# Kernel tuning notes

Measured on AMD Instinct MI355X. Metric: run time of the kernel, lower is better.

Reference implementation:

```python
import jax, jax.numpy as jnp
import numpy as np

D_ATT = 1024
N_HEADS = 16
D_HEAD = D_ATT // N_HEADS


def _xavier(key, shape, scale):
    # xavier_uniform for Linear(d, d): limit = sqrt(6/(fan_in+fan_out))
    limit = float(np.sqrt(6.0 / (shape[0] + shape[1])))
    return jax.random.uniform(key, shape, jnp.float32, -limit, limit) * scale


def setup_inputs() -> dict:
    key = jax.random.key(0)
    ks = jax.random.split(key, 7)
    B, Lt, Ls = 2, 2048, 2048
    s = 1.0 / np.sqrt(D_ATT)
    return {
        "x_target": jax.random.normal(ks[0], (B, Lt, D_ATT), jnp.float32),
        "x_source": jax.random.normal(ks[1], (B, Ls, D_ATT), jnp.float32),
        "Wq": _xavier(ks[2], (D_ATT, D_ATT), s),  # torch Linear weight [out, in]
        "Wk": _xavier(ks[3], (D_ATT, D_ATT), s),
        "Wv": _xavier(ks[4], (D_ATT, D_ATT), s),
        "Wo": _xavier(ks[5], (D_ATT, D_ATT), 1.0),
        "bo": jax.random.uniform(ks[6], (D_ATT,), jnp.float32, -s, s),
    }


def reference(x_target, x_source, Wq, Wk, Wv, Wo, bo):
    B, Lt, _ = x_target.shape
    Ls = x_source.shape[1]
    H, Dh = N_HEADS, D_HEAD
    # projections (torch Linear: x @ W^T); RoPE defaults to identity
    Q = (x_target @ Wq.T).reshape(B, Lt, H, Dh)  # [B, Lt, H, Dh]
    K = (x_source @ Wk.T).reshape(B, Ls, H, Dh)
    V = (x_source @ Wv.T).reshape(B, Ls, H, Dh)
    scores = jnp.einsum("bthd,bshd->bhts", Q, K) / np.sqrt(Dh)
    attn = jax.nn.softmax(scores, axis=-1)
    out = jnp.einsum("bhts,bshd->bthd", attn, V).reshape(B, Lt, H * Dh)
    return out @ Wo.T + bo  # dropout p=0 -> identity
```

## Files before the change

kernel.cpp:

```cpp
#include <hip/hip_runtime.h>
#include <hip/hip_bf16.h>

typedef short bf16x8 __attribute__((ext_vector_type(8)));
typedef float f32x4 __attribute__((ext_vector_type(4)));

#define LDP 72

__device__ __forceinline__ float bf2f(ushort u) {
    union { unsigned int i; float f; } v; v.i = ((unsigned int)u) << 16; return v.f;
}
__device__ __forceinline__ ushort f2bf(float f) {
    union { float f; unsigned int i; } v; v.f = f;
    unsigned int x = v.i;
    x += 0x7fffu + ((x >> 16) & 1u);
    return (ushort)(x >> 16);
}

#define MFMA(a, b, c) __builtin_amdgcn_mfma_f32_16x16x32_bf16(a, b, c, 0, 0, 0)

#define WAIT_BARRIER(N) asm volatile("s_waitcnt vmcnt(" #N ")\n\ts_barrier" ::: "memory")

__device__ __forceinline__ void gld_lds16(const ushort* g, ushort* l) {
    __builtin_amdgcn_global_load_lds(
        (const __attribute__((address_space(1))) unsigned int*)g,
        (__attribute__((address_space(3))) unsigned int*)l, 16, 0, 0);
}

#define WS_XT 0
#define WS_XS 4194304
#define WS_WQ 8388608
#define WS_WK 9437184
#define WS_WV 10485760
#define WS_WO 11534336
#define WS_QH 12582912
#define WS_KH 16777216
#define WS_VT 20971520
#define WS_AO 0

__global__ __launch_bounds__(256) void cast_bf16(
    const float* __restrict__ s0, const float* __restrict__ s1,
    const float* __restrict__ s2, const float* __restrict__ s3,
    const float* __restrict__ s4, const float* __restrict__ s5,
    ushort* __restrict__ ws)
{
    const int seg = blockIdx.y;
    const float* src = seg == 0 ? s0 : seg == 1 ? s1 : seg == 2 ? s2
                     : seg == 3 ? s3 : seg == 4 ? s4 : s5;
    const size_t off = seg == 0 ? WS_XT : seg == 1 ? WS_XS : seg == 2 ? WS_WQ
                     : seg == 3 ? WS_WK : seg == 4 ? WS_WV : (size_t)WS_WO;
    const int n4 = (seg < 2) ? 1048576 : 262144;
    ushort* d = ws + off;
    for (int i = blockIdx.x * 256 + threadIdx.x; i < n4; i += gridDim.x * 256) {
        float4 f = ((const float4*)src)[i];
        ushort4 u;
        u.x = f2bf(f.x); u.y = f2bf(f.y); u.z = f2bf(f.z); u.w = f2bf(f.w);
        ((ushort4*)d)[i] = u;
    }
}

__global__ __launch_bounds__(256) void gemm128(
    const ushort* __restrict__ xtb, const ushort* __restrict__ xsb,
    const ushort* __restrict__ wqb, const ushort* __restrict__ wkb,
    const ushort* __restrict__ wvb,
    ushort* __restrict__ qh, ushort* __restrict__ kh, ushort* __restrict__ vt)
{
    __shared__ __align__(16) ushort SM[24576];

    const int mode = blockIdx.z;
    const ushort* Ap = (mode == 0) ? xtb : xsb;
    const ushort* Wp = (mode == 0) ? wqb : (mode == 1 ? wkb : wvb);

    const int tid  = threadIdx.x;
    const int wave = tid >> 6, lane = tid & 63;
    const int quad = lane >> 4, lidx = lane & 15;
    const int wm = wave >> 1, wn = wave & 1;
    const int m0 = blockIdx.y * 128, n0 = blockIdx.x * 128;

    const int slr = lane >> 2, scb = lane & 3;
    auto stage = [&](int k0, int bufi) {
        ushort* Asb = SM + bufi * 4096;
        ushort* Bsb = SM + 12288 + bufi * 4096;
#pragma unroll
        for (int i2 = 0; i2 < 2; ++i2) {
            const int i = wave + i2 * 4;
            const int r = i * 16 + slr;
            gld_lds16(Ap + (size_t)(m0 + r) * 1024 + k0 + scb * 8, Asb + i * 512);
            gld_lds16(Wp + (size_t)(n0 + r) * 1024 + k0 + scb * 8, Bsb + i * 512);
        }
    };

    f32x4 acc[4][4] = {};
    stage(0, 0);
    stage(32, 1);

    for (int kt = 0; kt < 32; ++kt) {
        const int cur = kt % 3;
        WAIT_BARRIER(4);
        stage(((kt + 2) & 31) * 32, (kt + 2) % 3);
        const ushort* Asb = SM + cur * 4096;
        const ushort* Bsb = SM + 12288 + cur * 4096;
        bf16x8 af[4], bfr[4];
#pragma unroll
        for (int i = 0; i < 4; ++i) {
            af[i]  = *(const bf16x8*)(Asb + (wm * 64 + i * 16 + lidx) * 32 + quad * 8);
            bfr[i] = *(const bf16x8*)(Bsb + (wn * 64 + i * 16 + lidx) * 32 + quad * 8);
        }
#pragma unroll
        for (int mi = 0; mi < 4; ++mi)
#pragma unroll
            for (int ni = 0; ni < 4; ++ni)
                acc[mi][ni] = MFMA(af[mi], bfr[ni], acc[mi][ni]);
    }
    __syncthreads();

    ushort* scr = SM + wave * 4096;

    if (mode == 2) {
#pragma unroll
        for (int mi = 0; mi < 4; ++mi)
#pragma unroll
            for (int ni = 0; ni < 4; ++ni)
#pragma unroll
                for (int r = 0; r < 4; ++r) {
                    const int dl = ni * 16 + lidx;
                    const int tl = mi * 16 + quad * 4 + r;
                    const int col = (((tl >> 3) ^ (dl & 7)) << 3) | (tl & 7);
                    scr[dl * 64 + col] = f2bf(acc[mi][ni][r]);
                }
        asm volatile("s_waitcnt lgkmcnt(0)" ::: "memory");
        const int hh = (n0 + wn * 64) >> 6;
        const int bb = m0 >> 11;
        const int t0 = (m0 + wm * 64) & 2047;
        ushort* Vtp = vt + (size_t)(bb * 16 + hh) * 64 * 2048;
#pragma unroll
        for (int ii = 0; ii < 8; ++ii) {
            const int dl = ii * 8 + (lane >> 3);
            const int tb = lane & 7;
            uint4 vd = *(const uint4*)(scr + dl * 64 + ((tb ^ (dl & 7)) << 3));
            *(uint4*)(Vtp + (size_t)dl * 2048 + t0 + tb * 8) = vd;
        }
        return;
    }

#pragma unroll
    for (int mi = 0; mi < 4; ++mi)
#pragma unroll
        for (int ni = 0; ni < 4; ++ni)
#pragma unroll
            for (int r = 0; r < 4; ++r) {
                const int tl = mi * 16 + quad * 4 + r;
                const int dl = ni * 16 + lidx;
                const int col = (((dl >> 3) ^ (tl & 7)) << 3) | (dl & 7);
                scr[tl * 64 + col] = f2bf(acc[mi][ni][r]);
            }
    asm volatile("s_waitcnt lgkmcnt(0)" ::: "memory");
    {
        ushort* dst = (mode == 0) ? qh : kh;
        const int hh = (n0 + wn * 64) >> 6;
        const int bb = m0 >> 11;
        const int tbase = (m0 + wm * 64) & 2047;
        ushort* Hp = dst + (size_t)(bb * 16 + hh) * 2048 * 64;
#pragma unroll
        for (int ii = 0; ii < 8; ++ii) {
            const int tl = ii * 8 + (lane >> 3);
            const int c  = lane & 7;
            uint4 vd = *(const uint4*)(scr + tl * 64 + ((c ^ (tl & 7)) << 3));
            *(uint4*)(Hp + (size_t)(tbase + tl) * 64 + c * 8) = vd;
        }
    }
}

__global__ __launch_bounds__(256) void gemm_out(
    const ushort* __restrict__ aob, const ushort* __restrict__ wob,
    const float* __restrict__ bias, float* __restrict__ outf)
{
    __shared__ __align__(16) ushort SM[18432];

    const int tid  = threadIdx.x;
    const int wave = tid >> 6, lane = tid & 63;
    const int quad = lane >> 4, lidx = lane & 15;
    const int m0 = blockIdx.y * 128, n0 = blockIdx.x * 64;

    const int slr = lane >> 2, scb = lane & 3;
    auto stage = [&](int k0, int bufi) {
        ushort* Asb = SM + bufi * 4096;
        ushort* Bsb = SM + 12288 + bufi * 2048;
#pragma unroll
        for (int i2 = 0; i2 < 2; ++i2) {
            const int i = wave * 2 + i2;
            gld_lds16(aob + (size_t)(m0 + i * 16 + slr) * 1024 + k0 + scb * 8,
                      Asb + i * 512);
        }
        gld_lds16(wob + (size_t)(n0 + wave * 16 + slr) * 1024 + k0 + scb * 8,
                  Bsb + wave * 512);
    };

    f32x4 acc[2][4] = {};
    stage(0, 0);
    stage(32, 1);

    for (int kt = 0; kt < 32; ++kt) {
        const int cur = kt % 3;
        WAIT_BARRIER(3);
        stage(((kt + 2) & 31) * 32, (kt + 2) % 3);
        const ushort* Asb = SM + cur * 4096;
        const ushort* Bsb = SM + 12288 + cur * 2048;
        bf16x8 af[2], bfr[4];
#pragma unroll
        for (int i = 0; i < 2; ++i)
            af[i] = *(const bf16x8*)(Asb + (wave * 32 + i * 16 + lidx) * 32 + quad * 8);
#pragma unroll
        for (int i = 0; i < 4; ++i)
            bfr[i] = *(const bf16x8*)(Bsb + (i * 16 + lidx) * 32 + quad * 8);
#pragma unroll
        for (int mi = 0; mi < 2; ++mi)
#pragma unroll
            for (int ni = 0; ni < 4; ++ni)
                acc[mi][ni] = MFMA(af[mi], bfr[ni], acc[mi][ni]);
    }

#pragma unroll
    for (int mi = 0; mi < 2; ++mi)
#pragma unroll
        for (int ni = 0; ni < 4; ++ni)
#pragma unroll
            for (int r = 0; r < 4; ++r) {
                const int m = m0 + wave * 32 + mi * 16 + quad * 4 + r;
                const int n = n0 + ni * 16 + lidx;
                outf[(size_t)m * 1024 + n] = acc[mi][ni][r] + bias[n];
            }
}

__global__ __launch_bounds__(512) void flash_attn(
    const ushort* __restrict__ Qh, const ushort* __restrict__ Kh,
    const ushort* __restrict__ Vt, ushort* __restrict__ AO)
{
    __shared__ __align__(16) ushort Kb[3][4096];
    __shared__ __align__(16) ushort Vb[3][4096];
    __shared__ __align__(16) ushort P[8][16][LDP];

    const int tid  = threadIdx.x;
    const int wave = tid >> 6, lane = tid & 63;
    const int quad = lane >> 4, lidx = lane & 15;
    const int bh = blockIdx.y;
    const int b = bh >> 4, h = bh & 15;
    const int qbase = blockIdx.x * 128 + wave * 16;

    const ushort* Qp = Qh + (size_t)bh * 2048 * 64;
    const ushort* Kp = Kh + (size_t)bh * 2048 * 64;
    const ushort* Vp = Vt + (size_t)bh * 64 * 2048;

    bf16x8 q0, q1;
    {
        const ushort* qr = Qp + (size_t)(qbase + lidx) * 64 + quad * 8;
        union { ushort u[8]; uint4 v; } t0, t1;
        t0.v = *(const uint4*)qr;
        t1.v = *(const uint4*)(qr + 32);
#pragma unroll
        for (int i = 0; i < 8; ++i) {
            ((short*)&q0)[i] = (short)f2bf(bf2f(t0.u[i]) * 0.18033688f);
            ((short*)&q1)[i] = (short)f2bf(bf2f(t1.u[i]) * 0.18033688f);
        }
    }

    auto stage = [&](int s0, int bufi) {
        const int slot = wave * 64 + lane;
        const int r  = slot >> 3;
        const int bb = slot & 7;
        const int gb = bb ^ (r & 7);
        gld_lds16(Kp + (size_t)(s0 + r) * 64 + gb * 8, &Kb[bufi][wave * 512]);
        gld_lds16(Vp + (size_t)r * 2048 + s0 + gb * 8, &Vb[bufi][wave * 512]);
    };

    float lsum = 0.f;
    f32x4 o[4] = {};

    stage(0, 0);
    stage(64, 1);

    for (int j = 0; j < 32; ++j) {
        const int cur = j % 3;
        WAIT_BARRIER(2);
        stage(((j + 2) & 31) * 64, (j + 2) % 3);

        f32x4 s[4] = {};
#pragma unroll
        for (int n0 = 0; n0 < 4; ++n0) {
            const int row = n0 * 16 + lidx;
            bf16x8 kA = *(const bf16x8*)&Kb[cur][row * 64 + ((quad ^ (row & 7)) * 8)];
            bf16x8 kB = *(const bf16x8*)&Kb[cur][row * 64 + (((4 + quad) ^ (row & 7)) * 8)];
            s[n0] = MFMA(kA, q0, s[n0]);
            s[n0] = MFMA(kB, q1, s[n0]);
        }

        bf16x8 v0[4], v1[4];
#pragma unroll
        for (int n0 = 0; n0 < 4; ++n0) {
            const int d = n0 * 16 + lidx;
            v0[n0] = *(const bf16x8*)&Vb[cur][d * 64 + ((quad ^ (d & 7)) * 8)];
            v1[n0] = *(const bf16x8*)&Vb[cur][d * 64 + (((4 + quad) ^ (d & 7)) * 8)];
        }

#pragma unroll
        for (int n0 = 0; n0 < 4; ++n0) {
            float p0 = __builtin_amdgcn_exp2f(s[n0][0]);
            float p1 = __builtin_amdgcn_exp2f(s[n0][1]);
            float p2 = __builtin_amdgcn_exp2f(s[n0][2]);
            float p3 = __builtin_amdgcn_exp2f(s[n0][3]);
            lsum += (p0 + p1) + (p2 + p3);
            uint u0, u1;
            asm("v_cvt_pk_bf16_f32 %0, %1, %2" : "=v"(u0) : "v"(p0), "v"(p1));
            asm("v_cvt_pk_bf16_f32 %0, %1, %2" : "=v"(u1) : "v"(p2), "v"(p3));
            union { uint u[2]; uint2 v; } pw;
            pw.u[0] = u0; pw.u[1] = u1;
            *(uint2*)&P[wave][lidx][n0 * 16 + quad * 4] = pw.v;
        }
        asm volatile("s_waitcnt lgkmcnt(0)" ::: "memory");

        bf16x8 pA = *(const bf16x8*)&P[wave][lidx][quad * 8];
        bf16x8 pB = *(const bf16x8*)&P[wave][lidx][32 + quad * 8];

#pragma unroll
        for (int n0 = 0; n0 < 4; ++n0) {
            o[n0] = MFMA(pA, v0[n0], o[n0]);
            o[n0] = MFMA(pB, v1[n0], o[n0]);
        }
    }

    {
        float v = lsum;
        v += __shfl_xor(v, 16);
        v += __shfl_xor(v, 32);
        lsum = v;
    }
    float rs[4];
#pragma unroll
    for (int r = 0; r < 4; ++r)
        rs[r] = 1.0f / __shfl(lsum, quad * 4 + r);

#pragma unroll
    for (int n0 = 0; n0 < 4; ++n0)
#pragma unroll
        for (int r = 0; r < 4; ++r) {
            const int tt = qbase + quad * 4 + r;
            const int d  = n0 * 16 + lidx;
            AO[(size_t)(b * 2048 + tt) * 1024 + h * 64 + d] =
                f2bf(o[n0][r] * rs[r]);
        }
}

extern "C" void kernel_launch(void* const* d_in, const int* in_sizes, int n_in,
                              void* d_out, int out_size, void* d_ws, size_t ws_size,
                              hipStream_t stream) {
    const float* xt = (const float*)d_in[0];
    const float* xs = (const float*)d_in[1];
    const float* Wq = (const float*)d_in[2];
    const float* Wk = (const float*)d_in[3];
    const float* Wv = (const float*)d_in[4];
    const float* Wo = (const float*)d_in[5];
    const float* bo = (const float*)d_in[6];
    float* out = (float*)d_out;

    ushort* ws = (ushort*)d_ws;

    cast_bf16<<<dim3(1024, 6, 1), 256, 0, stream>>>(xt, xs, Wq, Wk, Wv, Wo, ws);

    gemm128<<<dim3(8, 32, 3), 256, 0, stream>>>(
        ws + WS_XT, ws + WS_XS, ws + WS_WQ, ws + WS_WK, ws + WS_WV,
        ws + WS_QH, ws + WS_KH, ws + WS_VT);

    flash_attn<<<dim3(16, 32, 1), 512, 0, stream>>>(
        ws + WS_QH, ws + WS_KH, ws + WS_VT, ws + WS_AO);

    gemm_out<<<dim3(16, 32, 1), 256, 0, stream>>>(
        ws + WS_AO, ws + WS_WO, bo, out);
}
```

Baseline: 201.8 us.

## Switch flash attention to 32x32x16 MFMA with in-register P via permlane32 swap

Rewrites the attention inner loop to use 32x32x16 bf16 MFMA tiles, giving each of four waves 32 query rows instead of eight waves with 16 rows each. The softmax probabilities are rearranged into the A-operand layout with permlane32_swap rather than a round trip through shared memory, which removes the P LDS buffer and its lgkm wait. The block shrinks to 256 threads and each thread issues two staging loads per buffer. The cost is higher register pressure from 16-wide accumulators and fewer waves per block to hide latency.

Result: no change. 202.2 us (+0.2%).

```diff
diff --git a/kernel.cpp b/kernel.cpp
--- a/kernel.cpp
+++ b/kernel.cpp
@@ -3,8 +3,8 @@
 
 typedef short bf16x8 __attribute__((ext_vector_type(8)));
 typedef float f32x4 __attribute__((ext_vector_type(4)));
-
-#define LDP 72
+typedef float f32x16 __attribute__((ext_vector_type(16)));
+typedef unsigned int uint2v __attribute__((ext_vector_type(2)));
 
 __device__ __forceinline__ float bf2f(ushort u) {
     union { unsigned int i; float f; } v; v.i = ((unsigned int)u) << 16; return v.f;
@@ -17,6 +17,7 @@
 }
 
 #define MFMA(a, b, c) __builtin_amdgcn_mfma_f32_16x16x32_bf16(a, b, c, 0, 0, 0)
+#define MFMA32(a, b, c) __builtin_amdgcn_mfma_f32_32x32x16_bf16(a, b, c, 0, 0, 0)
 
 #define WAIT_BARRIER(N) asm volatile("s_waitcnt vmcnt(" #N ")\n\ts_barrier" ::: "memory")
 
@@ -231,121 +232,128 @@
             }
 }
 
-__global__ __launch_bounds__(512) void flash_attn(
+__global__ __launch_bounds__(256) void flash_attn(
     const ushort* __restrict__ Qh, const ushort* __restrict__ Kh,
     const ushort* __restrict__ Vt, ushort* __restrict__ AO)
 {
     __shared__ __align__(16) ushort Kb[3][4096];
     __shared__ __align__(16) ushort Vb[3][4096];
-    __shared__ __align__(16) ushort P[8][16][LDP];
 
     const int tid  = threadIdx.x;
     const int wave = tid >> 6, lane = tid & 63;
-    const int quad = lane >> 4, lidx = lane & 15;
+    const int l31 = lane & 31, hf = lane >> 5;
     const int bh = blockIdx.y;
     const int b = bh >> 4, h = bh & 15;
-    const int qbase = blockIdx.x * 128 + wave * 16;
+    const int qbase = blockIdx.x * 128 + wave * 32;
 
     const ushort* Qp = Qh + (size_t)bh * 2048 * 64;
     const ushort* Kp = Kh + (size_t)bh * 2048 * 64;
     const ushort* Vp = Vt + (size_t)bh * 64 * 2048;
 
-    bf16x8 q0, q1;
-    {
-        const ushort* qr = Qp + (size_t)(qbase + lidx) * 64 + quad * 8;
-        union { ushort u[8]; uint4 v; } t0, t1;
-        t0.v = *(const uint4*)qr;
-        t1.v = *(const uint4*)(qr + 32);
-#pragma unroll
-        for (int i = 0; i < 8; ++i) {
-            ((short*)&q0)[i] = (short)f2bf(bf2f(t0.u[i]) * 0.18033688f);
-            ((short*)&q1)[i] = (short)f2bf(bf2f(t1.u[i]) * 0.18033688f);
-        }
+    bf16x8 q[4];
+#pragma unroll
+    for (int dblk = 0; dblk < 4; ++dblk) {
+        const ushort* qr = Qp + (size_t)(qbase + l31) * 64 + dblk * 16 + hf * 8;
+        union { ushort u[8]; uint4 v; } t;
+        t.v = *(const uint4*)qr;
+#pragma unroll
+        for (int i = 0; i < 8; ++i)
+            ((short*)&q[dblk])[i] = (short)f2bf(bf2f(t.u[i]) * 0.18033688f);
     }
 
     auto stage = [&](int s0, int bufi) {
-        const int slot = wave * 64 + lane;
-        const int r  = slot >> 3;
-        const int bb = slot & 7;
-        const int gb = bb ^ (r & 7);
-        gld_lds16(Kp + (size_t)(s0 + r) * 64 + gb * 8, &Kb[bufi][wave * 512]);
-        gld_lds16(Vp + (size_t)r * 2048 + s0 + gb * 8, &Vb[bufi][wave * 512]);
+#pragma unroll
+        for (int i = 0; i < 2; ++i) {
+            const int slot = i * 256 + wave * 64 + lane;
+            const int r  = slot >> 3;
+            const int bb = slot & 7;
+            const int gb = bb ^ (r & 7);
+            gld_lds16(Kp + (size_t)(s0 + r) * 64 + gb * 8,
+                      &Kb[bufi][i * 2048 + wave * 512]);
+            gld_lds16(Vp + (size_t)r * 2048 + s0 + gb * 8,
+                      &Vb[bufi][i * 2048 + wave * 512]);
+        }
     };
 
     float lsum = 0.f;
-    f32x4 o[4] = {};
+    f32x16 o[2] = {};
 
     stage(0, 0);
     stage(64, 1);
 
     for (int j = 0; j < 32; ++j) {
         const int cur = j % 3;
-        WAIT_BARRIER(2);
+        WAIT_BARRIER(4);
         stage(((j + 2) & 31) * 64, (j + 2) % 3);
 
-        f32x4 s[4] = {};
-#pragma unroll
-        for (int n0 = 0; n0 < 4; ++n0) {
-            const int row = n0 * 16 + lidx;
-            bf16x8 kA = *(const bf16x8*)&Kb[cur][row * 64 + ((quad ^ (row & 7)) * 8)];
-            bf16x8 kB = *(const bf16x8*)&Kb[cur][row * 64 + (((4 + quad) ^ (row & 7)) * 8)];
-            s[n0] = MFMA(kA, q0, s[n0]);
-            s[n0] = MFMA(kB, q1, s[n0]);
-        }
-
-        bf16x8 v0[4], v1[4];
-#pragma unroll
-        for (int n0 = 0; n0 < 4; ++n0) {
-            const int d = n0 * 16 + lidx;
-            v0[n0] = *(const bf16x8*)&Vb[cur][d * 64 + ((quad ^ (d & 7)) * 8)];
-            v1[n0] = *(const bf16x8*)&Vb[cur][d * 64 + (((4 + quad) ^ (d & 7)) * 8)];
-        }
-
-#pragma unroll
-        for (int n0 = 0; n0 < 4; ++n0) {
-            float p0 = __builtin_amdgcn_exp2f(s[n0][0]);
-            float p1 = __builtin_amdgcn_exp2f(s[n0][1]);
-            float p2 = __builtin_amdgcn_exp2f(s[n0][2]);
-            float p3 = __builtin_amdgcn_exp2f(s[n0][3]);
-            lsum += (p0 + p1) + (p2 + p3);
-            uint u0, u1;
-            asm("v_cvt_pk_bf16_f32 %0, %1, %2" : "=v"(u0) : "v"(p0), "v"(p1));
-            asm("v_cvt_pk_bf16_f32 %0, %1, %2" : "=v"(u1) : "v"(p2), "v"(p3));
-            union { uint u[2]; uint2 v; } pw;
-            pw.u[0] = u0; pw.u[1] = u1;
-            *(uint2*)&P[wave][lidx][n0 * 16 + quad * 4] = pw.v;
-        }
-        asm volatile("s_waitcnt lgkmcnt(0)" ::: "memory");
-
-        bf16x8 pA = *(const bf16x8*)&P[wave][lidx][quad * 8];
-        bf16x8 pB = *(const bf16x8*)&P[wave][lidx][32 + quad * 8];
-
-#pragma unroll
-        for (int n0 = 0; n0 < 4; ++n0) {
-            o[n0] = MFMA(pA, v0[n0], o[n0]);
-            o[n0] = MFMA(pB, v1[n0], o[n0]);
-        }
-    }
-
-    {
-        float v = lsum;
-        v += __shfl_xor(v, 16);
-        v += __shfl_xor(v, 32);
-        lsum = v;
-    }
-    float rs[4];
-#pragma unroll
-    for (int r = 0; r < 4; ++r)
-        rs[r] = 1.0f / __shfl(lsum, quad * 4 + r);
-
-#pragma unroll
-    for (int n0 = 0; n0 < 4; ++n0)
-#pragma unroll
-        for (int r = 0; r < 4; ++r) {
-            const int tt = qbase + quad * 4 + r;
-            const int d  = n0 * 16 + lidx;
+        f32x16 s[2] = {};
+#pragma unroll
+        for (int kb = 0; kb < 2; ++kb) {
+            const int row = kb * 32 + l31;
+#pragma unroll
+            for (int dblk = 0; dblk < 4; ++dblk) {
+                bf16x8 kf = *(const bf16x8*)
+                    &Kb[cur][row * 64 + (((dblk * 2 + hf) ^ (row & 7)) * 8)];
+                s[kb] = MFMA32(kf, q[dblk], s[kb]);
+            }
+        }
+
+        bf16x8 vf[2][4];
+#pragma unroll
+        for (int db = 0; db < 2; ++db) {
+            const int drow = db * 32 + l31;
+#pragma unroll
+            for (int c = 0; c < 4; ++c)
+                vf[db][c] = *(const bf16x8*)
+                    &Vb[cur][drow * 64 + (((c * 2 + hf) ^ (drow & 7)) * 8)];
+        }
+
+        uint W[2][4][2];
+#pragma unroll
+        for (int kb = 0; kb < 2; ++kb)
+#pragma unroll
+            for (int g = 0; g < 4; ++g) {
+                float p0 = __builtin_amdgcn_exp2f(s[kb][4 * g + 0]);
+                float p1 = __builtin_amdgcn_exp2f(s[kb][4 * g + 1]);
+                float p2 = __builtin_amdgcn_exp2f(s[kb][4 * g + 2]);
+                float p3 = __builtin_amdgcn_exp2f(s[kb][4 * g + 3]);
+                lsum += (p0 + p1) + (p2 + p3);
+                asm("v_cvt_pk_bf16_f32 %0, %1, %2"
+                    : "=v"(W[kb][g][0]) : "v"(p0), "v"(p1));
+                asm("v_cvt_pk_bf16_f32 %0, %1, %2"
+                    : "=v"(W[kb][g][1]) : "v"(p2), "v"(p3));
+            }
+
+#pragma unroll
+        for (int c = 0; c < 4; ++c) {
+            const int kb = c >> 1, gL = (c & 1) * 2;
+            uint2v r0 = __builtin_amdgcn_permlane32_swap(
+                W[kb][gL][0], W[kb][gL + 1][0], false, false);
+            uint2v r1 = __builtin_amdgcn_permlane32_swap(
+                W[kb][gL][1], W[kb][gL + 1][1], false, false);
+            union { uint u[4]; bf16x8 v; } A;
+            A.u[0] = r0[0]; A.u[1] = r1[0]; A.u[2] = r0[1]; A.u[3] = r1[1];
+            o[0] = MFMA32(A.v, vf[0][c], o[0]);
+            o[1] = MFMA32(A.v, vf[1][c], o[1]);
+        }
+    }
+
+    lsum += __shfl_xor(lsum, 32);
+    const float rcp = 1.0f / lsum;
+    float rs[16];
+#pragma unroll
+    for (int r = 0; r < 16; ++r)
+        rs[r] = __shfl(rcp, (r & 3) + 8 * (r >> 2) + 4 * hf);
+
+#pragma unroll
+    for (int db = 0; db < 2; ++db)
+#pragma unroll
+        for (int r = 0; r < 16; ++r) {
+            const int qq = (r & 3) + 8 * (r >> 2) + 4 * hf;
+            const int tt = qbase + qq;
+            const int d  = db * 32 + l31;
             AO[(size_t)(b * 2048 + tt) * 1024 + h * 64 + d] =
-                f2bf(o[n0][r] * rs[r]);
+                f2bf(o[db][r] * rs[r]);
         }
 }
 
@@ -369,7 +377,7 @@
         ws + WS_XT, ws + WS_XS, ws + WS_WQ, ws + WS_WK, ws + WS_WV,
         ws + WS_QH, ws + WS_KH, ws + WS_VT);
 
-    flash_attn<<<dim3(16, 32, 1), 512, 0, stream>>>(
+    flash_attn<<<dim3(16, 32, 1), 256, 0, stream>>>(
         ws + WS_QH, ws + WS_KH, ws + WS_VT, ws + WS_AO);
 
     gemm_out<<<dim3(16, 32, 1), 256, 0, stream>>>(
```
